# Kernel optimization log

Hardware: AMD Instinct MI355X
Metric: run time of the kernel (lower is better)

Reference implementation:

```python
import jax, jax.numpy as jnp
import numpy as np

N, E, G, F_IN, D = 50000, 400000, 256, 79, 400
BN_EPS = 1e-5


def setup_inputs() -> dict:
    key = jax.random.key(0)
    ks = jax.random.split(key, 16)
    w = lambda k, s: jax.random.normal(k, s, dtype=jnp.float32) * 0.05
    return {
        "x": jax.random.normal(ks[0], (N, F_IN), dtype=jnp.float32),
        "edge_index": jax.random.randint(ks[1], (2, E), 0, N, dtype=jnp.int32),
        "batch_index": jnp.sort(jax.random.randint(ks[2], (N,), 0, G, dtype=jnp.int32)),
        "num_graphs": G,
        "mlp1_w1": w(ks[3], (F_IN, D)), "mlp1_b1": jnp.zeros(D, jnp.float32),
        "mlp1_bn_g": jnp.ones(D, jnp.float32), "mlp1_bn_b": jnp.zeros(D, jnp.float32),
        "mlp1_bn_m": jnp.zeros(D, jnp.float32), "mlp1_bn_v": jnp.ones(D, jnp.float32),
        "mlp1_w2": w(ks[4], (D, D)), "mlp1_b2": jnp.zeros(D, jnp.float32),
        "mlp2_w1": w(ks[5], (D, D)), "mlp2_b1": jnp.zeros(D, jnp.float32),
        "mlp2_bn_g": jnp.ones(D, jnp.float32), "mlp2_bn_b": jnp.zeros(D, jnp.float32),
        "mlp2_bn_m": jnp.zeros(D, jnp.float32), "mlp2_bn_v": jnp.ones(D, jnp.float32),
        "mlp2_w2": w(ks[6], (D, D)), "mlp2_b2": jnp.zeros(D, jnp.float32),
        "out1_w": w(ks[7], (D, D)), "out1_b": jnp.zeros(D, jnp.float32),
        "out2_w": w(ks[8], (D, D)), "out2_b": jnp.zeros(D, jnp.float32),
        "out3_w": w(ks[9], (D, D)), "out3_b": jnp.zeros(D, jnp.float32),
        "out_w": w(ks[10], (2 * D, 1)), "out_b": jnp.zeros(1, jnp.float32),
        "eps1": jnp.full((1,), 5e-5, jnp.float32),
        "eps2": jnp.full((1,), 5e-5, jnp.float32),
        "eps3": jnp.full((1,), 5e-5, jnp.float32),
    }


def _bn(z, g, b, m, v):
    # BatchNorm1d in inference mode (running stats)
    return (z - m) * jax.lax.rsqrt(v + BN_EPS) * g + b


def _gin(h, src, dst, eps, w1, b1, g, bb, m, v, w2, b2):
    n = h.shape[0]
    agg = jax.ops.segment_sum(h[src], dst, num_segments=n)  # [N, d] scatter-add
    z = (1.0 + eps) * h + agg
    z = jax.nn.relu(_bn(z @ w1 + b1, g, bb, m, v))
    return jax.nn.relu(z @ w2 + b2)


def reference(x, edge_index, batch_index, num_graphs,
              mlp1_w1, mlp1_b1, mlp1_bn_g, mlp1_bn_b, mlp1_bn_m, mlp1_bn_v, mlp1_w2, mlp1_b2,
              mlp2_w1, mlp2_b1, mlp2_bn_g, mlp2_bn_b, mlp2_bn_m, mlp2_bn_v, mlp2_w2, mlp2_b2,
              out1_w, out1_b, out2_w, out2_b, out3_w, out3_b, out_w, out_b,
              eps1, eps2, eps3):
    src, dst = edge_index[0], edge_index[1]
    h = _gin(x, src, dst, eps1[0], mlp1_w1, mlp1_b1, mlp1_bn_g, mlp1_bn_b, mlp1_bn_m, mlp1_bn_v, mlp1_w2, mlp1_b2)
    h = jnp.tanh(h @ out1_w + out1_b)
    h = _gin(h, src, dst, eps2[0], mlp2_w1, mlp2_b1, mlp2_bn_g, mlp2_bn_b, mlp2_bn_m, mlp2_bn_v, mlp2_w2, mlp2_b2)
    h = jnp.tanh(h @ out2_w + out2_b)
    h = _gin(h, src, dst, eps3[0], mlp2_w1, mlp2_b1, mlp2_bn_g, mlp2_bn_b, mlp2_bn_m, mlp2_bn_v, mlp2_w2, mlp2_b2)
    h = jnp.tanh(h @ out3_w + out3_b)
    # dropout is identity in eval mode
    mx = jax.ops.segment_max(h, batch_index, num_segments=num_graphs)   # global_max_pool
    sm = jax.ops.segment_sum(h, batch_index, num_segments=num_graphs)
    cnt = jax.ops.segment_sum(jnp.ones((h.shape[0], 1), h.dtype), batch_index, num_segments=num_graphs)
    mn = sm / jnp.maximum(cnt, 1.0)                                      # global_mean_pool
    pooled = jnp.concatenate([mx, mn], axis=1)                           # [G, 2D]
    return pooled @ out_w + out_b
```

## Files before the change

### kernel.cpp

```cpp
#include <hip/hip_runtime.h>
#include <math.h>

#define NN 50000
#define NE 400000
#define NG 256
#define FIN 79
#define DD 400
#define LDK 448
#define LDK1 128
#define XP 80
#define NPAD 512
#define BK 64
#define MT ((NN + 127) / 128)
#define BN_EPS_F 1e-5f

#define SCAN_B 256
#define SCAN_NB ((NN + SCAN_B - 1) / SCAN_B)

typedef unsigned short u16;
typedef unsigned short ushort8 __attribute__((ext_vector_type(8)));
typedef unsigned short ushort4v __attribute__((ext_vector_type(4)));
typedef short short8 __attribute__((ext_vector_type(8)));
typedef float floatx4 __attribute__((ext_vector_type(4)));

__device__ inline u16 f2bf(float f) {
    unsigned int u = __builtin_bit_cast(unsigned int, f);
    u += 0x7fffu + ((u >> 16) & 1u);
    return (u16)(u >> 16);
}
__device__ inline float bf2f(u16 s) {
    unsigned int u = ((unsigned int)s) << 16;
    return __builtin_bit_cast(float, u);
}
__device__ inline float fast_tanh(float x) {
    float e = __expf(2.0f * x);
    return 1.0f - 2.0f / (e + 1.0f);
}

__global__ void k_gstart(const int* __restrict__ batch, int* __restrict__ gstart) {
    int g = blockIdx.x * blockDim.x + threadIdx.x;
    if (g > NG) return;
    int lo = 0, hi = NN;
    while (lo < hi) {
        int mid = (lo + hi) >> 1;
        if (batch[mid] < g) lo = mid + 1; else hi = mid;
    }
    gstart[g] = lo;
}

__global__ void k_zero_int(int* __restrict__ p, int n) {
    int i = blockIdx.x * blockDim.x + threadIdx.x;
    if (i < n) p[i] = 0;
}
__global__ void k_hist(const int* __restrict__ dst, int* __restrict__ deg) {
    int e = blockIdx.x * blockDim.x + threadIdx.x;
    if (e < NE) atomicAdd(&deg[dst[e]], 1);
}

__global__ void k_scan_a(const int* __restrict__ deg, int* __restrict__ bsum) {
    __shared__ int red[SCAN_B];
    int i = blockIdx.x * SCAN_B + threadIdx.x;
    red[threadIdx.x] = (i < NN) ? deg[i] : 0;
    __syncthreads();
    for (int s = SCAN_B / 2; s > 0; s >>= 1) {
        if (threadIdx.x < s) red[threadIdx.x] += red[threadIdx.x + s];
        __syncthreads();
    }
    if (threadIdx.x == 0) bsum[blockIdx.x] = red[0];
}
__global__ void k_scan_b(const int* __restrict__ bsum, int* __restrict__ boff) {
    __shared__ int buf[SCAN_B];
    int t = threadIdx.x;
    int v = (t < SCAN_NB) ? bsum[t] : 0;
    buf[t] = v;
    __syncthreads();
    for (int off = 1; off < SCAN_B; off <<= 1) {
        int add = (t >= off) ? buf[t - off] : 0;
        __syncthreads();
        buf[t] += add;
        __syncthreads();
    }
    if (t < SCAN_NB) boff[t] = buf[t] - v;
}
__global__ void k_scan_c(const int* __restrict__ deg, const int* __restrict__ boff,
                         int* __restrict__ rowptr, int* __restrict__ cursor) {
    __shared__ int buf[SCAN_B];
    int b = blockIdx.x;
    int i = b * SCAN_B + threadIdx.x;
    int v = (i < NN) ? deg[i] : 0;
    buf[threadIdx.x] = v;
    __syncthreads();
    for (int off = 1; off < SCAN_B; off <<= 1) {
        int add = (threadIdx.x >= off) ? buf[threadIdx.x - off] : 0;
        __syncthreads();
        buf[threadIdx.x] += add;
        __syncthreads();
    }
    int excl = boff[b] + buf[threadIdx.x] - v;
    if (i < NN) { rowptr[i] = excl; cursor[i] = excl; }
    if (b == 0 && threadIdx.x == 0) rowptr[NN] = NE;
}

__global__ void k_fill(const int* __restrict__ src, const int* __restrict__ dst,
                       int* __restrict__ cursor, int* __restrict__ eidx) {
    int e = blockIdx.x * blockDim.x + threadIdx.x;
    if (e < NE) {
        int pos = atomicAdd(&cursor[dst[e]], 1);
        eidx[pos] = src[e];
    }
}

__global__ void k_packw(const float* __restrict__ W, int K, u16* __restrict__ Wt, int ldk) {
    int idx = blockIdx.x * 256 + threadIdx.x;
    int total = NPAD * ldk;
    if (idx >= total) return;
    int n = idx / ldk, k = idx - n * ldk;
    float v = (n < DD && k < K) ? W[(size_t)k * DD + n] : 0.0f;
    Wt[idx] = f2bf(v);
}

__global__ __launch_bounds__(256)
void k_packx(const float* __restrict__ x, u16* __restrict__ xb) {
    int idx = blockIdx.x * 256 + threadIdx.x;
    if (idx >= NN * XP) return;
    int n = idx / XP, c = idx - n * XP;
    xb[idx] = (c < FIN) ? f2bf(x[(size_t)n * FIN + c]) : (u16)0;
}

__global__ __launch_bounds__(256)
void k_agg1(const u16* __restrict__ xb, const int* __restrict__ rowptr,
            const int* __restrict__ eidx, const float* __restrict__ eps,
            u16* __restrict__ z0) {
    int wave = threadIdx.x >> 6, lane = threadIdx.x & 63;
    int n = blockIdx.x * 4 + wave;
    if (lane >= 32) return;
    u16* zr = z0 + (size_t)n * LDK1;
    if (lane >= 20) {
        ushort4v zz = {0, 0, 0, 0};
        *(ushort4v*)&zr[XP + (lane - 20) * 4] = zz;
        return;
    }
    float s = 1.0f + eps[0];
    int c4 = lane * 4;
    ushort4v v = *(const ushort4v*)&xb[(size_t)n * XP + c4];
    float a[4];
    #pragma unroll
    for (int t = 0; t < 4; ++t) a[t] = s * bf2f(v[t]);
    int e0 = rowptr[n], e1 = rowptr[n + 1];
    int i = e0;
    for (; i + 2 <= e1; i += 2) {
        int s0 = eidx[i], s1 = eidx[i + 1];
        ushort4v v0 = *(const ushort4v*)&xb[(size_t)s0 * XP + c4];
        ushort4v v1 = *(const ushort4v*)&xb[(size_t)s1 * XP + c4];
        #pragma unroll
        for (int t = 0; t < 4; ++t) a[t] += bf2f(v0[t]) + bf2f(v1[t]);
    }
    if (i < e1) {
        int s0 = eidx[i];
        ushort4v v0 = *(const ushort4v*)&xb[(size_t)s0 * XP + c4];
        #pragma unroll
        for (int t = 0; t < 4; ++t) a[t] += bf2f(v0[t]);
    }
    ushort4v o;
    #pragma unroll
    for (int t = 0; t < 4; ++t) o[t] = f2bf(a[t]);
    *(ushort4v*)&zr[c4] = o;
}

__global__ __launch_bounds__(256)
void k_agg(const u16* __restrict__ h, const int* __restrict__ rowptr,
           const int* __restrict__ eidx, const float* __restrict__ eps,
           u16* __restrict__ z) {
    int wave = threadIdx.x >> 6, lane = threadIdx.x & 63;
    int n = blockIdx.x * 4 + wave;
    if (lane >= 50) return;
    float s = 1.0f + eps[0];
    int c8 = lane * 8;
    ushort8 v = *(const ushort8*)(h + (size_t)n * LDK + c8);
    float a[8];
    #pragma unroll
    for (int t = 0; t < 8; ++t) a[t] = s * bf2f(v[t]);
    int e0 = rowptr[n], e1 = rowptr[n + 1];
    int i = e0;
    for (; i + 2 <= e1; i += 2) {
        int s0 = eidx[i], s1 = eidx[i + 1];
        ushort8 v0 = *(const ushort8*)(h + (size_t)s0 * LDK + c8);
        ushort8 v1 = *(const ushort8*)(h + (size_t)s1 * LDK + c8);
        #pragma unroll
        for (int t = 0; t < 8; ++t) a[t] += bf2f(v0[t]) + bf2f(v1[t]);
    }
    if (i < e1) {
        int s0 = eidx[i];
        ushort8 v0 = *(const ushort8*)(h + (size_t)s0 * LDK + c8);
        #pragma unroll
        for (int t = 0; t < 8; ++t) a[t] += bf2f(v0[t]);
    }
    ushort8 o;
    #pragma unroll
    for (int t = 0; t < 8; ++t) o[t] = f2bf(a[t]);
    *(ushort8*)(z + (size_t)n * LDK + c8) = o;
}

#define CSTR 136
__global__ __launch_bounds__(256, 3)
void k_gemm(const u16* __restrict__ A, int lda, int ktiles,
            const u16* __restrict__ Wt,
            const float* __restrict__ bias,
            const float* __restrict__ bng, const float* __restrict__ bnb,
            const float* __restrict__ bnm, const float* __restrict__ bnv,
            u16* __restrict__ Y, int mode)
{
    __shared__ u16 smem[128 * CSTR];
    u16* As = smem;
    u16* Bs = smem + 128 * BK;
    u16* Cs = smem;

    int id = blockIdx.x;
    int mt = (id >> 5) * 8 + (id & 7);
    int nt = (id & 31) >> 3;
    if (mt >= MT) return;
    int m0 = mt * 128;
    int n0 = nt * 128;

    int tid = threadIdx.x;
    int wave = tid >> 6, lane = tid & 63;
    int wm = wave & 1, wn = wave >> 1;

    int srow = lane >> 3;
    int sc   = lane & 7;
    int swz  = (sc ^ srow) << 3;
    int lm = lane & 15;
    int q  = lane >> 4;

    bool nactive = (n0 + wn * 64) < LDK;

    const u16* gA[4]; const u16* gB[4];
    int lofs[4];
    #pragma unroll
    for (int j = 0; j < 4; ++j) {
        int rowL = wave * 32 + j * 8 + srow;
        lofs[j] = rowL * BK + swz;
        int gr = m0 + rowL; gr = gr < NN ? gr : NN - 1;
        gA[j] = A + (size_t)gr * lda + sc * 8;
        gB[j] = Wt + (size_t)(n0 + rowL) * lda + sc * 8;
    }

    ushort8 va[4], vb[4];
    #pragma unroll
    for (int j = 0; j < 4; ++j) { va[j] = *(const ushort8*)gA[j]; vb[j] = *(const ushort8*)gB[j]; }

    floatx4 acc[4][4] = {};

    for (int kt = 0; kt < ktiles; ++kt) {
        __syncthreads();
        #pragma unroll
        for (int j = 0; j < 4; ++j) {
            *(ushort8*)&As[lofs[j]] = va[j];
            *(ushort8*)&Bs[lofs[j]] = vb[j];
        }
        __syncthreads();
        if (kt + 1 < ktiles) {
            int ko = (kt + 1) * BK;
            #pragma unroll
            for (int j = 0; j < 4; ++j) {
                va[j] = *(const ushort8*)(gA[j] + ko);
                vb[j] = *(const ushort8*)(gB[j] + ko);
            }
        }
        if (nactive) {
            #pragma unroll
            for (int ks = 0; ks < 2; ++ks) {
                short8 af[4], bf[4];
                #pragma unroll
                for (int i = 0; i < 4; ++i) {
                    int r = wm * 64 + i * 16 + lm;
                    int ch = (ks * 4 + q) ^ (lm & 7);
                    af[i] = *(const short8*)&As[r * BK + ch * 8];
                }
                #pragma unroll
                for (int j = 0; j < 4; ++j) {
                    int r = wn * 64 + j * 16 + lm;
                    int ch = (ks * 4 + q) ^ (lm & 7);
                    bf[j] = *(const short8*)&Bs[r * BK + ch * 8];
                }
                #pragma unroll
                for (int i = 0; i < 4; ++i)
                    #pragma unroll
                    for (int j = 0; j < 4; ++j)
                        acc[i][j] = __builtin_amdgcn_mfma_f32_16x16x32_bf16(af[i], bf[j], acc[i][j], 0, 0, 0);
            }
        }
    }
    __syncthreads();

    #pragma unroll
    for (int j = 0; j < 4; ++j) {
        int nl = wn * 64 + j * 16 + lm;
        int n  = n0 + nl;
        bool live = n < DD;
        float bias_c = 0.0f, sc2 = 1.0f, sh = 0.0f;
        if (live) {
            bias_c = bias[n];
            if (mode == 0) {
                sc2 = bng[n] * rsqrtf(bnv[n] + BN_EPS_F);
                sh = bnb[n] - bnm[n] * sc2;
            }
        }
        #pragma unroll
        for (int i = 0; i < 4; ++i) {
            int rl = wm * 64 + i * 16 + q * 4;
            #pragma unroll
            for (int r = 0; r < 4; ++r) {
                u16 o = 0;
                if (live) {
                    float val = acc[i][j][r] + bias_c;
                    if (mode == 0)      val = fmaxf(fmaf(val, sc2, sh), 0.0f);
                    else if (mode == 1) val = fmaxf(val, 0.0f);
                    else                val = fast_tanh(val);
                    o = f2bf(val);
                }
                if (nactive) Cs[(rl + r) * CSTR + nl] = o;
            }
        }
    }
    __syncthreads();

    int row = tid >> 1, half = tid & 1;
    int m = m0 + row;
    if (m < NN) {
        #pragma unroll
        for (int k = 0; k < 8; ++k) {
            int coloff = half * 64 + k * 8;
            int n = n0 + coloff;
            if (n < LDK) {
                ushort8 v = *(const ushort8*)&Cs[row * CSTR + coloff];
                *(ushort8*)&Y[(size_t)m * LDK + n] = v;
            }
        }
    }
}

__global__ __launch_bounds__(256)
void k_pool(const u16* __restrict__ t3, const int* __restrict__ gstart,
            float* __restrict__ pooled) {
    __shared__ float smax[4][408];
    __shared__ float ssum[4][408];
    int g = blockIdx.x;
    int wave = threadIdx.x >> 6, lane = threadIdx.x & 63;
    int s = gstart[g], e = gstart[g + 1];
    if (lane < 50) {
        int c8 = lane * 8;
        float mx[8], sm[8];
        #pragma unroll
        for (int t = 0; t < 8; ++t) { mx[t] = -INFINITY; sm[t] = 0.0f; }
        for (int n = s + wave; n < e; n += 4) {
            ushort8 v = *(const ushort8*)&t3[(size_t)n * LDK + c8];
            #pragma unroll
            for (int t = 0; t < 8; ++t) {
                float f = bf2f(v[t]);
                mx[t] = fmaxf(mx[t], f);
                sm[t] += f;
            }
        }
        #pragma unroll
        for (int t = 0; t < 8; ++t) {
            smax[wave][c8 + t] = mx[t];
            ssum[wave][c8 + t] = sm[t];
        }
    }
    __syncthreads();
    float cnt = fmaxf((float)(e - s), 1.0f);
    for (int c = threadIdx.x; c < DD; c += 256) {
        float m = fmaxf(fmaxf(smax[0][c], smax[1][c]), fmaxf(smax[2][c], smax[3][c]));
        float su = ssum[0][c] + ssum[1][c] + ssum[2][c] + ssum[3][c];
        pooled[(size_t)g * 2 * DD + c] = m;
        pooled[(size_t)g * 2 * DD + DD + c] = su / cnt;
    }
}

__global__ void k_final(const float* __restrict__ pooled, const float* __restrict__ w,
                        const float* __restrict__ b, float* __restrict__ out) {
    __shared__ float red[256];
    int g = blockIdx.x;
    float p = 0.0f;
    for (int j = threadIdx.x; j < 2 * DD; j += blockDim.x)
        p += pooled[(size_t)g * 2 * DD + j] * w[j];
    red[threadIdx.x] = p;
    __syncthreads();
    for (int s = 128; s > 0; s >>= 1) {
        if (threadIdx.x < s) red[threadIdx.x] += red[threadIdx.x + s];
        __syncthreads();
    }
    if (threadIdx.x == 0) out[g] = red[0] + b[0];
}

extern "C" void kernel_launch(void* const* d_in, const int* in_sizes, int n_in,
                              void* d_out, int out_size, void* d_ws, size_t ws_size,
                              hipStream_t stream) {
    const float* x     = (const float*)d_in[0];
    const int*   ei    = (const int*)d_in[1];
    const int*   batch = (const int*)d_in[2];
    const float* m1w1  = (const float*)d_in[4];
    const float* m1b1  = (const float*)d_in[5];
    const float* m1g   = (const float*)d_in[6];
    const float* m1bb  = (const float*)d_in[7];
    const float* m1m   = (const float*)d_in[8];
    const float* m1v   = (const float*)d_in[9];
    const float* m1w2  = (const float*)d_in[10];
    const float* m1b2  = (const float*)d_in[11];
    const float* m2w1  = (const float*)d_in[12];
    const float* m2b1  = (const float*)d_in[13];
    const float* m2g   = (const float*)d_in[14];
    const float* m2bb  = (const float*)d_in[15];
    const float* m2m   = (const float*)d_in[16];
    const float* m2v   = (const float*)d_in[17];
    const float* m2w2  = (const float*)d_in[18];
    const float* m2b2  = (const float*)d_in[19];
    const float* o1w   = (const float*)d_in[20];
    const float* o1b   = (const float*)d_in[21];
    const float* o2w   = (const float*)d_in[22];
    const float* o2b   = (const float*)d_in[23];
    const float* o3w   = (const float*)d_in[24];
    const float* o3b   = (const float*)d_in[25];
    const float* ow    = (const float*)d_in[26];
    const float* ob    = (const float*)d_in[27];
    const float* eps1  = (const float*)d_in[28];
    const float* eps2  = (const float*)d_in[29];
    const float* eps3  = (const float*)d_in[30];
    const int* srcI = ei;
    const int* dstI = ei + NE;

    u16* buf1 = (u16*)d_ws;
    u16* buf2 = buf1 + (size_t)NN * LDK;
    u16* buf3 = buf2 + (size_t)NN * LDK;
    u16* z0   = buf3 + (size_t)NN * LDK;
    u16* w1t  = z0 + (size_t)NN * LDK1;
    u16* m1w2t = w1t + (size_t)NPAD * LDK1;
    u16* m2w1t = m1w2t + (size_t)NPAD * LDK;
    u16* m2w2t = m2w1t + (size_t)NPAD * LDK;
    u16* o1t   = m2w2t + (size_t)NPAD * LDK;
    u16* o2t   = o1t + (size_t)NPAD * LDK;
    u16* o3t   = o2t + (size_t)NPAD * LDK;
    u16* xb    = o3t + (size_t)NPAD * LDK;
    float* pooled = (float*)(xb + (size_t)NN * XP);
    int* gstart = (int*)(pooled + (size_t)NG * 2 * DD);
    int* rowptr = gstart + (NG + 2);
    int* cursor = rowptr + (NN + 1);
    int* deg    = cursor + NN;
    int* eidx   = deg + NN;
    int* bsum   = eidx + NE;
    int* boff   = bsum + SCAN_NB;

    float* out = (float*)d_out;

    int gemmBlocks = ((MT + 7) / 8) * 32;

    k_gstart<<<2, 256, 0, stream>>>(batch, gstart);
    k_zero_int<<<(NN + 255) / 256, 256, 0, stream>>>(deg, NN);
    k_hist<<<(NE + 255) / 256, 256, 0, stream>>>(dstI, deg);
    k_scan_a<<<SCAN_NB, SCAN_B, 0, stream>>>(deg, bsum);
    k_scan_b<<<1, SCAN_B, 0, stream>>>(bsum, boff);
    k_scan_c<<<SCAN_NB, SCAN_B, 0, stream>>>(deg, boff, rowptr, cursor);
    k_fill<<<(NE + 255) / 256, 256, 0, stream>>>(srcI, dstI, cursor, eidx);

    int pw1 = (NPAD * LDK1 + 255) / 256;
    int pw = (NPAD * LDK + 255) / 256;
    k_packw<<<pw1, 256, 0, stream>>>(m1w1, FIN, w1t, LDK1);
    k_packw<<<pw, 256, 0, stream>>>(m1w2, DD, m1w2t, LDK);
    k_packw<<<pw, 256, 0, stream>>>(m2w1, DD, m2w1t, LDK);
    k_packw<<<pw, 256, 0, stream>>>(m2w2, DD, m2w2t, LDK);
    k_packw<<<pw, 256, 0, stream>>>(o1w, DD, o1t, LDK);
    k_packw<<<pw, 256, 0, stream>>>(o2w, DD, o2t, LDK);
    k_packw<<<pw, 256, 0, stream>>>(o3w, DD, o3t, LDK);
    k_packx<<<(NN * XP + 255) / 256, 256, 0, stream>>>(x, xb);

    k_agg1<<<NN / 4, 256, 0, stream>>>(xb, rowptr, eidx, eps1, z0);
    k_gemm<<<gemmBlocks, 256, 0, stream>>>(z0, LDK1, LDK1 / BK, w1t, m1b1,
                                           m1g, m1bb, m1m, m1v, buf1, 0);
    k_gemm<<<gemmBlocks, 256, 0, stream>>>(buf1, LDK, LDK / BK, m1w2t, m1b2,
                                           nullptr, nullptr, nullptr, nullptr, buf2, 1);
    k_gemm<<<gemmBlocks, 256, 0, stream>>>(buf2, LDK, LDK / BK, o1t, o1b,
                                           nullptr, nullptr, nullptr, nullptr, buf3, 2);

    k_agg<<<NN / 4, 256, 0, stream>>>(buf3, rowptr, eidx, eps2, buf1);
    k_gemm<<<gemmBlocks, 256, 0, stream>>>(buf1, LDK, LDK / BK, m2w1t, m2b1,
                                           m2g, m2bb, m2m, m2v, buf2, 0);
    k_gemm<<<gemmBlocks, 256, 0, stream>>>(buf2, LDK, LDK / BK, m2w2t, m2b2,
                                           nullptr, nullptr, nullptr, nullptr, buf1, 1);
    k_gemm<<<gemmBlocks, 256, 0, stream>>>(buf1, LDK, LDK / BK, o2t, o2b,
                                           nullptr, nullptr, nullptr, nullptr, buf2, 2);

    k_agg<<<NN / 4, 256, 0, stream>>>(buf2, rowptr, eidx, eps3, buf1);
    k_gemm<<<gemmBlocks, 256, 0, stream>>>(buf1, LDK, LDK / BK, m2w1t, m2b1,
                                           m2g, m2bb, m2m, m2v, buf3, 0);
    k_gemm<<<gemmBlocks, 256, 0, stream>>>(buf3, LDK, LDK / BK, m2w2t, m2b2,
                                           nullptr, nullptr, nullptr, nullptr, buf1, 1);
    k_gemm<<<gemmBlocks, 256, 0, stream>>>(buf1, LDK, LDK / BK, o3t, o3b,
                                           nullptr, nullptr, nullptr, nullptr, buf3, 2);

    k_pool<<<NG, 256, 0, stream>>>(buf3, gstart, pooled);
    k_final<<<NG, 256, 0, stream>>>(pooled, ow, ob, out);
}
```

Before: 876.1 us.

## Restructure GEMM to full-width 64-row tiles with A staged in LDS

Replaces the 128x128 tiled GEMM with a kernel where each block loads a full 64-row slab of A (all K) into LDS once. Each wave computes 112 output columns, streaming weight fragments directly from global/L2 into registers with double buffering. This removes the per-k-tile LDS staging and barriers, and the reloading of A for each of the four N tiles. The cost is higher register pressure (28 accumulators), a larger LDS footprint that limits occupancy to 2 blocks, and unswizzled weight reads served from cache.

```diff
diff --git a/kernel.cpp b/kernel.cpp
--- a/kernel.cpp
+++ b/kernel.cpp
@@ -9,9 +9,8 @@
 #define LDK 448
 #define LDK1 128
 #define XP 80
-#define NPAD 512
-#define BK 64
-#define MT ((NN + 127) / 128)
+#define NPAD 448
+#define ZSTR 456
 #define BN_EPS_F 1e-5f
 
 #define SCAN_B 256
@@ -201,102 +200,70 @@
     *(ushort8*)(z + (size_t)n * LDK + c8) = o;
 }
 
-#define CSTR 136
-__global__ __launch_bounds__(256, 3)
-void k_gemm(const u16* __restrict__ A, int lda, int ktiles,
-            const u16* __restrict__ Wt,
-            const float* __restrict__ bias,
-            const float* __restrict__ bng, const float* __restrict__ bnb,
-            const float* __restrict__ bnm, const float* __restrict__ bnv,
-            u16* __restrict__ Y, int mode)
+template<int LDA, int KT>
+__global__ __launch_bounds__(256, 2)
+void k_gemm_t(const u16* __restrict__ A,
+              const u16* __restrict__ Wt,
+              const float* __restrict__ bias,
+              const float* __restrict__ bng, const float* __restrict__ bnb,
+              const float* __restrict__ bnm, const float* __restrict__ bnv,
+              u16* __restrict__ Y, int mode)
 {
-    __shared__ u16 smem[128 * CSTR];
-    u16* As = smem;
-    u16* Bs = smem + 128 * BK;
-    u16* Cs = smem;
-
-    int id = blockIdx.x;
-    int mt = (id >> 5) * 8 + (id & 7);
-    int nt = (id & 31) >> 3;
-    if (mt >= MT) return;
-    int m0 = mt * 128;
-    int n0 = nt * 128;
+    constexpr int KC = LDA / 8;
+    constexpr int CH = (64 * KC) / 256;
+    __shared__ u16 zin[64 * ZSTR];
 
     int tid = threadIdx.x;
+    int m0 = blockIdx.x * 64;
+
+    #pragma unroll
+    for (int c = 0; c < CH; ++c) {
+        int chunk = tid + c * 256;
+        int row = chunk / KC, col8 = chunk - row * KC;
+        int gr = m0 + row; gr = gr < NN ? gr : NN - 1;
+        ushort8 v = *(const ushort8*)&A[(size_t)gr * LDA + col8 * 8];
+        *(ushort8*)&zin[row * ZSTR + col8 * 8] = v;
+    }
+    __syncthreads();
+
     int wave = tid >> 6, lane = tid & 63;
-    int wm = wave & 1, wn = wave >> 1;
-
-    int srow = lane >> 3;
-    int sc   = lane & 7;
-    int swz  = (sc ^ srow) << 3;
-    int lm = lane & 15;
-    int q  = lane >> 4;
-
-    bool nactive = (n0 + wn * 64) < LDK;
-
-    const u16* gA[4]; const u16* gB[4];
-    int lofs[4];
-    #pragma unroll
-    for (int j = 0; j < 4; ++j) {
-        int rowL = wave * 32 + j * 8 + srow;
-        lofs[j] = rowL * BK + swz;
-        int gr = m0 + rowL; gr = gr < NN ? gr : NN - 1;
-        gA[j] = A + (size_t)gr * lda + sc * 8;
-        gB[j] = Wt + (size_t)(n0 + rowL) * lda + sc * 8;
-    }
-
-    ushort8 va[4], vb[4];
-    #pragma unroll
-    for (int j = 0; j < 4; ++j) { va[j] = *(const ushort8*)gA[j]; vb[j] = *(const ushort8*)gB[j]; }
-
-    floatx4 acc[4][4] = {};
-
-    for (int kt = 0; kt < ktiles; ++kt) {
-        __syncthreads();
-        #pragma unroll
-        for (int j = 0; j < 4; ++j) {
-            *(ushort8*)&As[lofs[j]] = va[j];
-            *(ushort8*)&Bs[lofs[j]] = vb[j];
-        }
-        __syncthreads();
-        if (kt + 1 < ktiles) {
-            int ko = (kt + 1) * BK;
+    int lm = lane & 15, q = lane >> 4;
+    int ncol0 = wave * 112;
+
+    const u16* wbase[7];
+    #pragma unroll
+    for (int j = 0; j < 7; ++j)
+        wbase[j] = Wt + (size_t)(ncol0 + j * 16 + lm) * LDA + q * 8;
+    const u16* abase = &zin[lm * ZSTR + q * 8];
+
+    floatx4 acc[4][7] = {};
+    short8 regB[2][7], regA[2][4];
+    #pragma unroll
+    for (int j = 0; j < 7; ++j) regB[0][j] = *(const short8*)wbase[j];
+    #pragma unroll
+    for (int i = 0; i < 4; ++i) regA[0][i] = *(const short8*)(abase + i * 16 * ZSTR);
+
+    for (int kt = 0; kt < KT; ++kt) {
+        int cur = kt & 1, nxt = cur ^ 1;
+        if (kt + 1 < KT) {
+            int ko = (kt + 1) * 32;
             #pragma unroll
-            for (int j = 0; j < 4; ++j) {
-                va[j] = *(const ushort8*)(gA[j] + ko);
-                vb[j] = *(const ushort8*)(gB[j] + ko);
-            }
-        }
-        if (nactive) {
+            for (int j = 0; j < 7; ++j) regB[nxt][j] = *(const short8*)(wbase[j] + ko);
             #pragma unroll
-            for (int ks = 0; ks < 2; ++ks) {
-                short8 af[4], bf[4];
-                #pragma unroll
-                for (int i = 0; i < 4; ++i) {
-                    int r = wm * 64 + i * 16 + lm;
-                    int ch = (ks * 4 + q) ^ (lm & 7);
-                    af[i] = *(const short8*)&As[r * BK + ch * 8];
-                }
-                #pragma unroll
-                for (int j = 0; j < 4; ++j) {
-                    int r = wn * 64 + j * 16 + lm;
-                    int ch = (ks * 4 + q) ^ (lm & 7);
-                    bf[j] = *(const short8*)&Bs[r * BK + ch * 8];
-                }
-                #pragma unroll
-                for (int i = 0; i < 4; ++i)
-                    #pragma unroll
-                    for (int j = 0; j < 4; ++j)
-                        acc[i][j] = __builtin_amdgcn_mfma_f32_16x16x32_bf16(af[i], bf[j], acc[i][j], 0, 0, 0);
-            }
-        }
-    }
-    __syncthreads();
-
-    #pragma unroll
-    for (int j = 0; j < 4; ++j) {
-        int nl = wn * 64 + j * 16 + lm;
-        int n  = n0 + nl;
+            for (int i = 0; i < 4; ++i) regA[nxt][i] = *(const short8*)(abase + i * 16 * ZSTR + ko);
+        }
+        #pragma unroll
+        for (int i = 0; i < 4; ++i)
+            #pragma unroll
+            for (int j = 0; j < 7; ++j)
+                acc[i][j] = __builtin_amdgcn_mfma_f32_16x16x32_bf16(regA[cur][i], regB[cur][j], acc[i][j], 0, 0, 0);
+    }
+    __syncthreads();
+
+    u16* Cs = zin;
+    #pragma unroll
+    for (int j = 0; j < 7; ++j) {
+        int n = ncol0 + j * 16 + lm;
         bool live = n < DD;
         float bias_c = 0.0f, sc2 = 1.0f, sh = 0.0f;
         if (live) {
@@ -308,7 +275,7 @@
         }
         #pragma unroll
         for (int i = 0; i < 4; ++i) {
-            int rl = wm * 64 + i * 16 + q * 4;
+            int rl = i * 16 + q * 4;
             #pragma unroll
             for (int r = 0; r < 4; ++r) {
                 u16 o = 0;
@@ -319,23 +286,20 @@
                     else                val = fast_tanh(val);
                     o = f2bf(val);
                 }
-                if (nactive) Cs[(rl + r) * CSTR + nl] = o;
+                Cs[(rl + r) * ZSTR + n] = o;
             }
         }
     }
     __syncthreads();
 
-    int row = tid >> 1, half = tid & 1;
-    int m = m0 + row;
-    if (m < NN) {
-        #pragma unroll
-        for (int k = 0; k < 8; ++k) {
-            int coloff = half * 64 + k * 8;
-            int n = n0 + coloff;
-            if (n < LDK) {
-                ushort8 v = *(const ushort8*)&Cs[row * CSTR + coloff];
-                *(ushort8*)&Y[(size_t)m * LDK + n] = v;
-            }
+    #pragma unroll
+    for (int c = 0; c < 14; ++c) {
+        int chunk = tid + c * 256;
+        int row = chunk / 56, col8 = chunk - row * 56;
+        int m = m0 + row;
+        if (m < NN) {
+            ushort8 v = *(const ushort8*)&Cs[row * ZSTR + col8 * 8];
+            *(ushort8*)&Y[(size_t)m * LDK + col8 * 8] = v;
         }
     }
 }
@@ -453,7 +417,7 @@
 
     float* out = (float*)d_out;
 
-    int gemmBlocks = ((MT + 7) / 8) * 32;
+    int gemmBlocks = (NN + 63) / 64;
 
     k_gstart<<<2, 256, 0, stream>>>(batch, gstart);
     k_zero_int<<<(NN + 255) / 256, 256, 0, stream>>>(deg, NN);
@@ -475,27 +439,27 @@
     k_packx<<<(NN * XP + 255) / 256, 256, 0, stream>>>(x, xb);
 
     k_agg1<<<NN / 4, 256, 0, stream>>>(xb, rowptr, eidx, eps1, z0);
-    k_gemm<<<gemmBlocks, 256, 0, stream>>>(z0, LDK1, LDK1 / BK, w1t, m1b1,
+    k_gemm_t<LDK1, LDK1 / 32><<<gemmBlocks, 256, 0, stream>>>(z0, w1t, m1b1,
                                            m1g, m1bb, m1m, m1v, buf1, 0);
-    k_gemm<<<gemmBlocks, 256, 0, stream>>>(buf1, LDK, LDK / BK, m1w2t, m1b2,
+    k_gemm_t<LDK, LDK / 32><<<gemmBlocks, 256, 0, stream>>>(buf1, m1w2t, m1b2,
                                            nullptr, nullptr, nullptr, nullptr, buf2, 1);
-    k_gemm<<<gemmBlocks, 256, 0, stream>>>(buf2, LDK, LDK / BK, o1t, o1b,
+    k_gemm_t<LDK, LDK / 32><<<gemmBlocks, 256, 0, stream>>>(buf2, o1t, o1b,
                                            nullptr, nullptr, nullptr, nullptr, buf3, 2);
 
     k_agg<<<NN / 4, 256, 0, stream>>>(buf3, rowptr, eidx, eps2, buf1);
-    k_gemm<<<gemmBlocks, 256, 0, stream>>>(buf1, LDK, LDK / BK, m2w1t, m2b1,
+    k_gemm_t<LDK, LDK / 32><<<gemmBlocks, 256, 0, stream>>>(buf1, m2w1t, m2b1,
                                            m2g, m2bb, m2m, m2v, buf2, 0);
-    k_gemm<<<gemmBlocks, 256, 0, stream>>>(buf2, LDK, LDK / BK, m2w2t, m2b2,
+    k_gemm_t<LDK, LDK / 32><<<gemmBlocks, 256, 0, stream>>>(buf2, m2w2t, m2b2,
                                            nullptr, nullptr, nullptr, nullptr, buf1, 1);
-    k_gemm<<<gemmBlocks, 256, 0, stream>>>(buf1, LDK, LDK / BK, o2t, o2b,
+    k_gemm_t<LDK, LDK / 32><<<gemmBlocks, 256, 0, stream>>>(buf1, o2t, o2b,
                                            nullptr, nullptr, nullptr, nullptr, buf2, 2);
 
     k_agg<<<NN / 4, 256, 0, stream>>>(buf2, rowptr, eidx, eps3, buf1);
-    k_gemm<<<gemmBlocks, 256, 0, stream>>>(buf1, LDK, LDK / BK, m2w1t, m2b1,
+    k_gemm_t<LDK, LDK / 32><<<gemmBlocks, 256, 0, stream>>>(buf1, m2w1t, m2b1,
                                            m2g, m2bb, m2m, m2v, buf3, 0);
-    k_gemm<<<gemmBlocks, 256, 0, stream>>>(buf3, LDK, LDK / BK, m2w2t, m2b2,
+    k_gemm_t<LDK, LDK / 32><<<gemmBlocks, 256, 0, stream>>>(buf3, m2w2t, m2b2,
                                            nullptr, nullptr, nullptr, nullptr, buf1, 1);
-    k_gemm<<<gemmBlocks, 256, 0, stream>>>(buf1, LDK, LDK / BK, o3t, o3b,
+    k_gemm_t<LDK, LDK / 32><<<gemmBlocks, 256, 0, stream>>>(buf1, o3t, o3b,
                                            nullptr, nullptr, nullptr, nullptr, buf3, 2);
 
     k_pool<<<NG, 256, 0, stream>>>(buf3, gstart, pooled);
```

Result: slower. 1.088 ms (+24.2%).
